# Kernel optimization log

Hardware: AMD Instinct MI355X
Metric: run time of the kernel (lower is better)

The kernel has to match this reference:

```python
import jax, jax.numpy as jnp
import numpy as np

B, N, T, H = 16, 512, 100, 64

def setup_inputs() -> dict:
    key = jax.random.key(0)
    ks = jax.random.split(key, 9)
    s = 0.1
    return {
        "x": jax.random.normal(ks[0], (B, N, T), dtype=jnp.float32),
        "conv1_w": jax.random.normal(ks[1], (16, 1, 3), dtype=jnp.float32) * s,
        "conv1_b": jax.random.normal(ks[2], (16,), dtype=jnp.float32) * s,
        "conv2_w": jax.random.normal(ks[3], (32, 16, 3), dtype=jnp.float32) * s,
        "conv2_b": jax.random.normal(ks[4], (32,), dtype=jnp.float32) * s,
        "W_ih": jax.random.normal(ks[5], (3 * H, 32), dtype=jnp.float32) * s,
        "W_hh": jax.random.normal(ks[6], (3 * H, H), dtype=jnp.float32) * s,
        "b_ih": jax.random.normal(ks[7], (3 * H,), dtype=jnp.float32) * s,
        "b_hh": jax.random.normal(ks[8], (3 * H,), dtype=jnp.float32) * s,
    }

def _causal_conv_relu(h, w, b):
    # h: [BN, C_in, T]; left-pad (k-1)*dilation = 2 for causality
    y = jax.lax.conv_general_dilated(
        h, w, window_strides=(1,), padding=[(2, 0)],
        dimension_numbers=("NCH", "OIH", "NCH"))
    return jax.nn.relu(y + b[None, :, None])

def reference(x, conv1_w, conv1_b, conv2_w, conv2_b, W_ih, W_hh, b_ih, b_hh):
    b_, n_, t_ = x.shape
    h = x.reshape(b_ * n_, 1, t_)
    h = _causal_conv_relu(h, conv1_w, conv1_b)   # [BN, 16, T]
    h = _causal_conv_relu(h, conv2_w, conv2_b)   # [BN, 32, T]
    seq = h.transpose(0, 2, 1)                   # [BN, T, 32]
    # precompute input-to-gate projections for all timesteps: [BN, T, 3H]
    xp = jnp.einsum("btc,gc->btg", seq, W_ih) + b_ih
    hdim = W_hh.shape[1]

    def step(hprev, xt):
        gh = hprev @ W_hh.T + b_hh               # [BN, 3H]
        xr, xz, xn = jnp.split(xt, 3, axis=-1)
        hr, hz, hn = jnp.split(gh, 3, axis=-1)
        r = jax.nn.sigmoid(xr + hr)
        z = jax.nn.sigmoid(xz + hz)
        nn_ = jnp.tanh(xn + r * hn)
        hnew = (1.0 - z) * nn_ + z * hprev
        return hnew, None

    h0 = jnp.zeros((b_ * n_, hdim), dtype=x.dtype)
    hf, _ = jax.lax.scan(step, h0, xp.transpose(1, 0, 2))  # scan over T
    return hf.reshape(b_, n_, hdim)
```

## Files before the change

### kernel.cpp

```cpp
#include <hip/hip_runtime.h>
#include <stdint.h>

typedef __attribute__((ext_vector_type(8))) short s16x8;
typedef __attribute__((ext_vector_type(4))) float f32x4;

__device__ __forceinline__ short f2bf(float f){
  union { float f; uint32_t u; } v; v.f = f;
  uint32_t u = v.u;
  u += 0x7fffu + ((u >> 16) & 1u);
  return (short)(u >> 16);
}
__device__ __forceinline__ float sigm_fast(float x){
  float e = __builtin_amdgcn_exp2f(x * -1.44269504f);
  return __builtin_amdgcn_rcpf(1.f + e);
}
__device__ __forceinline__ float tanh_fast(float x){
  float e = __builtin_amdgcn_exp2f(x * 2.88539008f);
  return __builtin_fmaf(-2.f, __builtin_amdgcn_rcpf(e + 1.f), 1.f);
}

#define MFMA16(a, b, c) __builtin_amdgcn_mfma_f32_16x16x32_bf16((a), (b), (c), 0, 0, 0)

__global__ __launch_bounds__(256, 2) void te_fused(
    const float* __restrict__ x,
    const float* __restrict__ w1, const float* __restrict__ b1,
    const float* __restrict__ w2, const float* __restrict__ b2,
    const float* __restrict__ Wih, const float* __restrict__ Whh,
    const float* __restrict__ bih, const float* __restrict__ bhh,
    float* __restrict__ out)
{
  constexpr int T = 100;
  constexpr int M = 16;
  __shared__ float x_s[M * T];
  __shared__ short hA[2][16 * 72];
  __shared__ short ring[4][16 * 24];
  __shared__ short s_s[2][16 * 40];

  const int tid  = threadIdx.x;
  const int lane = tid & 63;
  const int wv   = tid >> 6;
  const int l15  = lane & 15;
  const int lg   = lane >> 4;
  const int seq0 = blockIdx.x * M;
  const int sl   = tid >> 4;
  const int chc  = tid & 15;

  {
    const float4* gx = reinterpret_cast<const float4*>(x + (size_t)seq0 * T);
    float4* sx = reinterpret_cast<float4*>(x_s);
    for (int i = tid; i < (M * T) / 4; i += 256) sx[i] = gx[i];
  }
  {
    int* p = reinterpret_cast<int*>(&hA[0][0]);
    for (int i = tid; i < (16 * 72) / 2; i += 256) p[i] = 0;
    int* q = reinterpret_cast<int*>(&ring[0][0]);
    for (int i = tid; i < (4 * 16 * 24) / 2; i += 256) q[i] = 0;
  }

  s16x8 WhhHi[3][2], WihHi[3];
  f32x4 bias_r, bias_z, bias_xn, bias_hn;
#pragma unroll
  for (int g = 0; g < 3; ++g) {
    const int n = 64 * g + 16 * wv + l15;
#pragma unroll
    for (int ks = 0; ks < 2; ++ks) {
      const float* p = Whh + n * 64 + ks * 32 + lg * 8;
#pragma unroll
      for (int j = 0; j < 8; ++j) WhhHi[g][ks][j] = f2bf(p[j]);
    }
    const float* q = Wih + n * 32 + lg * 8;
#pragma unroll
    for (int j = 0; j < 8; ++j) WihHi[g][j] = f2bf(q[j]);
    float bi = bih[n], bh = bhh[n];
    if (g == 0) { float v = bi + bh; bias_r  = (f32x4){v, v, v, v}; }
    if (g == 1) { float v = bi + bh; bias_z  = (f32x4){v, v, v, v}; }
    if (g == 2) { bias_xn = (f32x4){bi, bi, bi, bi};
                  bias_hn = (f32x4){bh, bh, bh, bh}; }
  }

  s16x8 cW2[2];
  f32x4 b2v4;
  {
    const int nt = wv & 1;
    const int ch = 16 * nt + l15;
    float bv = b2[ch];
    b2v4 = (f32x4){bv, bv, bv, bv};
#pragma unroll
    for (int ks = 0; ks < 2; ++ks) {
      s16x8 h8;
#pragma unroll
      for (int j = 0; j < 8; ++j) {
        const int k = ks * 32 + lg * 8 + j;
        const int g = k >> 4, ii = k & 15;
        h8[j] = (g < 3) ? f2bf(w2[ch * 48 + ii * 3 + g]) : (short)0;
      }
      cW2[ks] = h8;
    }
  }

  const float w1v0 = w1[chc * 3 + 0], w1v1 = w1[chc * 3 + 1], w1v2 = w1[chc * 3 + 2];
  const float b1v = b1[chc];

  __syncthreads();

  float xa_r = x_s[sl * T + 0];
  float xb_r = x_s[sl * T + 1];

  const int i0a = (lg & 1) * 8;
  const int grp = lg >> 1;

  auto conv2_step = [&](int u, int buf) {
    const int sA0 = (u + 2 + grp) & 3;
    const int sA1 = (u + grp) & 3;
    s16x8 a0 = *reinterpret_cast<const s16x8*>(&ring[sA0][l15 * 24 + i0a]);
    s16x8 a1 = *reinterpret_cast<const s16x8*>(&ring[sA1][l15 * 24 + i0a]);
    f32x4 sa = MFMA16(a1, cW2[1], MFMA16(a0, cW2[0], b2v4));
    short* sw = &s_s[buf][0];
    float m0 = sa[0] > 0.f ? sa[0] : 0.f;
    float m1 = sa[1] > 0.f ? sa[1] : 0.f;
    float m2 = sa[2] > 0.f ? sa[2] : 0.f;
    float m3 = sa[3] > 0.f ? sa[3] : 0.f;
    uint32_t u01, u23;
    asm("v_cvt_pk_bf16_f32 %0, %1, %2" : "=v"(u01) : "v"(m0), "v"(m1));
    asm("v_cvt_pk_bf16_f32 %0, %1, %2" : "=v"(u23) : "v"(m2), "v"(m3));
    const int cbase = (wv & 1) * 16 + l15;
    sw[(lg * 4 + 0) * 40 + cbase] = (short)(u01 & 0xffff);
    sw[(lg * 4 + 1) * 40 + cbase] = (short)(u01 >> 16);
    sw[(lg * 4 + 2) * 40 + cbase] = (short)(u23 & 0xffff);
    sw[(lg * 4 + 3) * 40 + cbase] = (short)(u23 >> 16);
  };

  {
    float c = b1v + w1v2 * xa_r;
    c = c > 0.f ? c : 0.f;
    uint32_t cu;
    asm("v_cvt_pk_bf16_f32 %0, %1, %2" : "=v"(cu) : "v"(c), "v"(c));
    ring[0][sl * 24 + chc] = (short)(cu & 0xffff);
  }
  __syncthreads();
  if (wv < 2) conv2_step(0, 0);
  {
    float c = b1v + w1v1 * xa_r + w1v2 * xb_r;
    c = c > 0.f ? c : 0.f;
    uint32_t cu;
    asm("v_cvt_pk_bf16_f32 %0, %1, %2" : "=v"(cu) : "v"(c), "v"(c));
    ring[1][sl * 24 + chc] = (short)(cu & 0xffff);
  }
  __syncthreads();

  float hreg[4] = {0.f, 0.f, 0.f, 0.f};

  for (int t = 0; t < T; ++t) {
    s16x8 as_ = *reinterpret_cast<const s16x8*>(&s_s[t & 1][l15 * 40 + lg * 8]);
    const short* hb = &hA[t & 1][0];
    const int ho = l15 * 72 + lg * 8;
    s16x8 ah0 = *reinterpret_cast<const s16x8*>(hb + ho);
    s16x8 ah1 = *reinterpret_cast<const s16x8*>(hb + ho + 32);

    f32x4 pre_r = MFMA16(as_, WihHi[0],
                  MFMA16(ah1, WhhHi[0][1],
                  MFMA16(ah0, WhhHi[0][0], bias_r)));
    f32x4 pre_z = MFMA16(as_, WihHi[1],
                  MFMA16(ah1, WhhHi[1][1],
                  MFMA16(ah0, WhhHi[1][0], bias_z)));
    f32x4 xn = MFMA16(as_, WihHi[2], bias_xn);
    f32x4 hn = MFMA16(ah1, WhhHi[2][1],
               MFMA16(ah0, WhhHi[2][0], bias_hn));

    if (t < T - 1 && wv < 2) conv2_step(t + 1, (t + 1) & 1);

    if (t < T - 2) {
      float xc = x_s[sl * T + t + 2];
      float c = b1v + w1v0 * xa_r + w1v1 * xb_r + w1v2 * xc;
      c = c > 0.f ? c : 0.f;
      uint32_t cu;
      asm("v_cvt_pk_bf16_f32 %0, %1, %2" : "=v"(cu) : "v"(c), "v"(c));
      ring[(t + 2) & 3][sl * 24 + chc] = (short)(cu & 0xffff);
      xa_r = xb_r; xb_r = xc;
    }

    float hnew[4];
#pragma unroll
    for (int i2 = 0; i2 < 4; ++i2) {
      float r = sigm_fast(pre_r[i2]);
      float z = sigm_fast(pre_z[i2]);
      float arg = __builtin_fmaf(r, hn[i2], xn[i2]);
      float tn = tanh_fast(arg);
      float h = __builtin_fmaf(z, hreg[i2] - tn, tn);
      hreg[i2] = h;
      hnew[i2] = h;
    }
    short* hw = &hA[(t + 1) & 1][0];
    uint32_t p01, p23;
    asm("v_cvt_pk_bf16_f32 %0, %1, %2" : "=v"(p01) : "v"(hnew[0]), "v"(hnew[1]));
    asm("v_cvt_pk_bf16_f32 %0, %1, %2" : "=v"(p23) : "v"(hnew[2]), "v"(hnew[3]));
    const int hbase = 16 * wv + l15;
    hw[(lg * 4 + 0) * 72 + hbase] = (short)(p01 & 0xffff);
    hw[(lg * 4 + 1) * 72 + hbase] = (short)(p01 >> 16);
    hw[(lg * 4 + 2) * 72 + hbase] = (short)(p23 & 0xffff);
    hw[(lg * 4 + 3) * 72 + hbase] = (short)(p23 >> 16);
    __syncthreads();
  }

#pragma unroll
  for (int i2 = 0; i2 < 4; ++i2) {
    out[(size_t)(seq0 + lg * 4 + i2) * 64 + 16 * wv + l15] = hreg[i2];
  }
}

extern "C" void kernel_launch(void* const* d_in, const int* in_sizes, int n_in,
                              void* d_out, int out_size, void* d_ws, size_t ws_size,
                              hipStream_t stream)
{
  (void)in_sizes; (void)n_in; (void)d_ws; (void)ws_size; (void)out_size;
  const float* x   = (const float*)d_in[0];
  const float* w1  = (const float*)d_in[1];
  const float* b1  = (const float*)d_in[2];
  const float* w2  = (const float*)d_in[3];
  const float* b2  = (const float*)d_in[4];
  const float* Wih = (const float*)d_in[5];
  const float* Whh = (const float*)d_in[6];
  const float* bih = (const float*)d_in[7];
  const float* bhh = (const float*)d_in[8];
  float* out = (float*)d_out;
  te_fused<<<512, 256, 0, stream>>>(x, w1, b1, w2, b2, Wih, Whh, bih, bhh, out);
}
```

Measured before the change: 79.83 us.

## Unroll GRU loop by four, split conv work across waves, add MFMA priority

Unrolls the recurrent time loop by four so ring, h and s buffer offsets become compile-time constants, removing per-step index math and branch overhead. Conv1 work moves to waves 2-3 (two sequences per thread, packed bf16 convert) and conv2 stays on waves 0-1, so each wave does less side work on the critical path. Raises wave priority around the MFMA chain with s_setprio. The change adds code size and relies on precomputed offset arrays staying in registers.

```diff
diff --git a/kernel.cpp b/kernel.cpp
--- a/kernel.cpp
+++ b/kernel.cpp
@@ -42,8 +42,6 @@
   const int l15  = lane & 15;
   const int lg   = lane >> 4;
   const int seq0 = blockIdx.x * M;
-  const int sl   = tid >> 4;
-  const int chc  = tid & 15;
 
   {
     const float4* gx = reinterpret_cast<const float4*>(x + (size_t)seq0 * T);
@@ -81,8 +79,7 @@
   s16x8 cW2[2];
   f32x4 b2v4;
   {
-    const int nt = wv & 1;
-    const int ch = 16 * nt + l15;
+    const int ch = 16 * (wv & 1) + l15;
     float bv = b2[ch];
     b2v4 = (f32x4){bv, bv, bv, bv};
 #pragma unroll
@@ -98,109 +95,135 @@
     }
   }
 
-  const float w1v0 = w1[chc * 3 + 0], w1v1 = w1[chc * 3 + 1], w1v2 = w1[chc * 3 + 2];
-  const float b1v = b1[chc];
-
-  __syncthreads();
-
-  float xa_r = x_s[sl * T + 0];
-  float xb_r = x_s[sl * T + 1];
+  const int cidx = tid & 127;
+  const int csl  = cidx >> 4;
+  const int cch  = cidx & 15;
+  const float w1v0 = w1[cch * 3 + 0], w1v1 = w1[cch * 3 + 1], w1v2 = w1[cch * 3 + 2];
+  const float b1v = b1[cch];
 
   const int i0a = (lg & 1) * 8;
   const int grp = lg >> 1;
-
-  auto conv2_step = [&](int u, int buf) {
-    const int sA0 = (u + 2 + grp) & 3;
-    const int sA1 = (u + grp) & 3;
-    s16x8 a0 = *reinterpret_cast<const s16x8*>(&ring[sA0][l15 * 24 + i0a]);
-    s16x8 a1 = *reinterpret_cast<const s16x8*>(&ring[sA1][l15 * 24 + i0a]);
-    f32x4 sa = MFMA16(a1, cW2[1], MFMA16(a0, cW2[0], b2v4));
-    short* sw = &s_s[buf][0];
-    float m0 = sa[0] > 0.f ? sa[0] : 0.f;
-    float m1 = sa[1] > 0.f ? sa[1] : 0.f;
-    float m2 = sa[2] > 0.f ? sa[2] : 0.f;
-    float m3 = sa[3] > 0.f ? sa[3] : 0.f;
-    uint32_t u01, u23;
-    asm("v_cvt_pk_bf16_f32 %0, %1, %2" : "=v"(u01) : "v"(m0), "v"(m1));
-    asm("v_cvt_pk_bf16_f32 %0, %1, %2" : "=v"(u23) : "v"(m2), "v"(m3));
-    const int cbase = (wv & 1) * 16 + l15;
-    sw[(lg * 4 + 0) * 40 + cbase] = (short)(u01 & 0xffff);
-    sw[(lg * 4 + 1) * 40 + cbase] = (short)(u01 >> 16);
-    sw[(lg * 4 + 2) * 40 + cbase] = (short)(u23 & 0xffff);
-    sw[(lg * 4 + 3) * 40 + cbase] = (short)(u23 >> 16);
-  };
-
-  {
-    float c = b1v + w1v2 * xa_r;
-    c = c > 0.f ? c : 0.f;
+  const short* ringRdBase = &ring[0][0] + l15 * 24 + i0a;
+  int sA0off[4], sA1off[4];
+#pragma unroll
+  for (int p = 0; p < 4; ++p) {
+    sA0off[p] = ((p + 3 + grp) & 3) * 384;
+    sA1off[p] = ((p + 1 + grp) & 3) * 384;
+  }
+  const short* sRdBase = &s_s[0][0] + l15 * 40 + lg * 8;
+  const short* hRdBase = &hA[0][0] + l15 * 72 + lg * 8;
+  short* hWrBase = &hA[0][0] + (lg * 4) * 72 + 16 * wv + l15;
+  short* swWr    = &s_s[0][0] + (lg * 4) * 40 + (wv & 1) * 16 + l15;
+  short* ringWrA = &ring[0][0] + csl * 24 + cch;
+  short* ringWrB = &ring[0][0] + (csl + 8) * 24 + cch;
+  const float* xpA = &x_s[csl * T];
+  const float* xpB = &x_s[(csl + 8) * T];
+
+  __syncthreads();
+
+#define CONV2_STEP(P_, WB_) do {                                              \
+    s16x8 a0 = *reinterpret_cast<const s16x8*>(ringRdBase + sA0off[(P_)]);    \
+    s16x8 a1 = *reinterpret_cast<const s16x8*>(ringRdBase + sA1off[(P_)]);    \
+    f32x4 sa = MFMA16(a1, cW2[1], MFMA16(a0, cW2[0], b2v4));                  \
+    float m0 = sa[0] > 0.f ? sa[0] : 0.f;                                     \
+    float m1 = sa[1] > 0.f ? sa[1] : 0.f;                                     \
+    float m2 = sa[2] > 0.f ? sa[2] : 0.f;                                     \
+    float m3 = sa[3] > 0.f ? sa[3] : 0.f;                                     \
+    uint32_t u01, u23;                                                        \
+    asm("v_cvt_pk_bf16_f32 %0, %1, %2" : "=v"(u01) : "v"(m0), "v"(m1));       \
+    asm("v_cvt_pk_bf16_f32 %0, %1, %2" : "=v"(u23) : "v"(m2), "v"(m3));       \
+    swWr[(WB_) * 640 +   0] = (short)(u01 & 0xffff);                          \
+    swWr[(WB_) * 640 +  40] = (short)(u01 >> 16);                             \
+    swWr[(WB_) * 640 +  80] = (short)(u23 & 0xffff);                          \
+    swWr[(WB_) * 640 + 120] = (short)(u23 >> 16);                             \
+  } while (0)
+
+  float xaA = 0.f, xbA = 0.f, xaB = 0.f, xbB = 0.f;
+  if (wv >= 2) {
+    xaA = xpA[0]; xbA = xpA[1];
+    xaB = xpB[0]; xbB = xpB[1];
+    float cA = b1v + w1v2 * xaA; cA = cA > 0.f ? cA : 0.f;
+    float cB = b1v + w1v2 * xaB; cB = cB > 0.f ? cB : 0.f;
     uint32_t cu;
-    asm("v_cvt_pk_bf16_f32 %0, %1, %2" : "=v"(cu) : "v"(c), "v"(c));
-    ring[0][sl * 24 + chc] = (short)(cu & 0xffff);
+    asm("v_cvt_pk_bf16_f32 %0, %1, %2" : "=v"(cu) : "v"(cA), "v"(cB));
+    ringWrA[0] = (short)(cu & 0xffff);
+    ringWrB[0] = (short)(cu >> 16);
   }
   __syncthreads();
-  if (wv < 2) conv2_step(0, 0);
-  {
-    float c = b1v + w1v1 * xa_r + w1v2 * xb_r;
-    c = c > 0.f ? c : 0.f;
+  if (wv < 2) CONV2_STEP(3, 0);
+  if (wv >= 2) {
+    float cA = b1v + w1v1 * xaA + w1v2 * xbA; cA = cA > 0.f ? cA : 0.f;
+    float cB = b1v + w1v1 * xaB + w1v2 * xbB; cB = cB > 0.f ? cB : 0.f;
     uint32_t cu;
-    asm("v_cvt_pk_bf16_f32 %0, %1, %2" : "=v"(cu) : "v"(c), "v"(c));
-    ring[1][sl * 24 + chc] = (short)(cu & 0xffff);
+    asm("v_cvt_pk_bf16_f32 %0, %1, %2" : "=v"(cu) : "v"(cA), "v"(cB));
+    ringWrA[384] = (short)(cu & 0xffff);
+    ringWrB[384] = (short)(cu >> 16);
   }
   __syncthreads();
 
   float hreg[4] = {0.f, 0.f, 0.f, 0.f};
 
-  for (int t = 0; t < T; ++t) {
-    s16x8 as_ = *reinterpret_cast<const s16x8*>(&s_s[t & 1][l15 * 40 + lg * 8]);
-    const short* hb = &hA[t & 1][0];
-    const int ho = l15 * 72 + lg * 8;
-    s16x8 ah0 = *reinterpret_cast<const s16x8*>(hb + ho);
-    s16x8 ah1 = *reinterpret_cast<const s16x8*>(hb + ho + 32);
-
-    f32x4 pre_r = MFMA16(as_, WihHi[0],
-                  MFMA16(ah1, WhhHi[0][1],
-                  MFMA16(ah0, WhhHi[0][0], bias_r)));
-    f32x4 pre_z = MFMA16(as_, WihHi[1],
-                  MFMA16(ah1, WhhHi[1][1],
-                  MFMA16(ah0, WhhHi[1][0], bias_z)));
-    f32x4 xn = MFMA16(as_, WihHi[2], bias_xn);
-    f32x4 hn = MFMA16(ah1, WhhHi[2][1],
-               MFMA16(ah0, WhhHi[2][0], bias_hn));
-
-    if (t < T - 1 && wv < 2) conv2_step(t + 1, (t + 1) & 1);
-
-    if (t < T - 2) {
-      float xc = x_s[sl * T + t + 2];
-      float c = b1v + w1v0 * xa_r + w1v1 * xb_r + w1v2 * xc;
-      c = c > 0.f ? c : 0.f;
-      uint32_t cu;
-      asm("v_cvt_pk_bf16_f32 %0, %1, %2" : "=v"(cu) : "v"(c), "v"(c));
-      ring[(t + 2) & 3][sl * 24 + chc] = (short)(cu & 0xffff);
-      xa_r = xb_r; xb_r = xc;
-    }
-
-    float hnew[4];
-#pragma unroll
-    for (int i2 = 0; i2 < 4; ++i2) {
-      float r = sigm_fast(pre_r[i2]);
-      float z = sigm_fast(pre_z[i2]);
-      float arg = __builtin_fmaf(r, hn[i2], xn[i2]);
-      float tn = tanh_fast(arg);
-      float h = __builtin_fmaf(z, hreg[i2] - tn, tn);
-      hreg[i2] = h;
-      hnew[i2] = h;
-    }
-    short* hw = &hA[(t + 1) & 1][0];
-    uint32_t p01, p23;
-    asm("v_cvt_pk_bf16_f32 %0, %1, %2" : "=v"(p01) : "v"(hnew[0]), "v"(hnew[1]));
-    asm("v_cvt_pk_bf16_f32 %0, %1, %2" : "=v"(p23) : "v"(hnew[2]), "v"(hnew[3]));
-    const int hbase = 16 * wv + l15;
-    hw[(lg * 4 + 0) * 72 + hbase] = (short)(p01 & 0xffff);
-    hw[(lg * 4 + 1) * 72 + hbase] = (short)(p01 >> 16);
-    hw[(lg * 4 + 2) * 72 + hbase] = (short)(p23 & 0xffff);
-    hw[(lg * 4 + 3) * 72 + hbase] = (short)(p23 >> 16);
-    __syncthreads();
-  }
+#define GRU_STEP(T_, P_, C2_, C1_) do {                                       \
+    const int rb_ = (P_) & 1, wb_ = rb_ ^ 1;                                  \
+    s16x8 as_ = *reinterpret_cast<const s16x8*>(sRdBase + rb_ * 640);         \
+    s16x8 ah0 = *reinterpret_cast<const s16x8*>(hRdBase + rb_ * 1152);        \
+    s16x8 ah1 = *reinterpret_cast<const s16x8*>(hRdBase + rb_ * 1152 + 32);   \
+    __builtin_amdgcn_s_setprio(1);                                            \
+    f32x4 pre_r = MFMA16(as_, WihHi[0],                                       \
+                  MFMA16(ah1, WhhHi[0][1],                                    \
+                  MFMA16(ah0, WhhHi[0][0], bias_r)));                         \
+    f32x4 pre_z = MFMA16(as_, WihHi[1],                                       \
+                  MFMA16(ah1, WhhHi[1][1],                                    \
+                  MFMA16(ah0, WhhHi[1][0], bias_z)));                         \
+    f32x4 xn = MFMA16(as_, WihHi[2], bias_xn);                                \
+    f32x4 hn = MFMA16(ah1, WhhHi[2][1],                                       \
+               MFMA16(ah0, WhhHi[2][0], bias_hn));                            \
+    __builtin_amdgcn_s_setprio(0);                                            \
+    if ((C2_) && wv < 2) { CONV2_STEP((P_), wb_); }                           \
+    if ((C1_) && wv >= 2) {                                                   \
+      float xcA = xpA[(T_) + 2], xcB = xpB[(T_) + 2];                         \
+      float cA = b1v + w1v0 * xaA + w1v1 * xbA + w1v2 * xcA;                  \
+      cA = cA > 0.f ? cA : 0.f;                                               \
+      float cB = b1v + w1v0 * xaB + w1v1 * xbB + w1v2 * xcB;                  \
+      cB = cB > 0.f ? cB : 0.f;                                               \
+      uint32_t cu_;                                                           \
+      asm("v_cvt_pk_bf16_f32 %0, %1, %2" : "=v"(cu_) : "v"(cA), "v"(cB));     \
+      ringWrA[(((P_) + 2) & 3) * 384] = (short)(cu_ & 0xffff);                \
+      ringWrB[(((P_) + 2) & 3) * 384] = (short)(cu_ >> 16);                   \
+      xaA = xbA; xbA = xcA; xaB = xbB; xbB = xcB;                             \
+    }                                                                         \
+    float hnew[4];                                                            \
+    _Pragma("unroll")                                                         \
+    for (int i2 = 0; i2 < 4; ++i2) {                                          \
+      float r = sigm_fast(pre_r[i2]);                                         \
+      float z = sigm_fast(pre_z[i2]);                                         \
+      float arg = __builtin_fmaf(r, hn[i2], xn[i2]);                          \
+      float tn = tanh_fast(arg);                                              \
+      float h = __builtin_fmaf(z, hreg[i2] - tn, tn);                         \
+      hreg[i2] = h;                                                           \
+      hnew[i2] = h;                                                           \
+    }                                                                         \
+    uint32_t p01, p23;                                                        \
+    asm("v_cvt_pk_bf16_f32 %0, %1, %2" : "=v"(p01) : "v"(hnew[0]), "v"(hnew[1])); \
+    asm("v_cvt_pk_bf16_f32 %0, %1, %2" : "=v"(p23) : "v"(hnew[2]), "v"(hnew[3])); \
+    hWrBase[wb_ * 1152 +   0] = (short)(p01 & 0xffff);                        \
+    hWrBase[wb_ * 1152 +  72] = (short)(p01 >> 16);                           \
+    hWrBase[wb_ * 1152 + 144] = (short)(p23 & 0xffff);                        \
+    hWrBase[wb_ * 1152 + 216] = (short)(p23 >> 16);                           \
+    __syncthreads();                                                          \
+  } while (0)
+
+#pragma unroll 1
+  for (int t = 0; t < 96; t += 4) {
+    GRU_STEP(t + 0, 0, true, true);
+    GRU_STEP(t + 1, 1, true, true);
+    GRU_STEP(t + 2, 2, true, true);
+    GRU_STEP(t + 3, 3, true, true);
+  }
+  GRU_STEP(96, 0, true, true);
+  GRU_STEP(97, 1, true, true);
+  GRU_STEP(98, 2, true, false);
+  GRU_STEP(99, 3, false, false);
 
 #pragma unroll
   for (int i2 = 0; i2 < 4; ++i2) {
```

Result: faster. 74.11 us (-7.2%).

## Batch conv stages in 16-step chunks ahead of the GRU recurrence

Applied to the files above, without the earlier changes.

Replaces the per-timestep interleaved conv1/conv2 pipeline with chunked precomputation: every 16 timesteps, conv1 outputs for the chunk are written to shared memory, then all four waves compute conv2 for the chunk via MFMA, and then 16 fully unrolled GRU steps run using only the precomputed inputs. This takes conv work off the serial recurrence's critical path and adds s_setprio around the gate MFMAs. In exchange it uses much more LDS (about 27 KB more per block), which may reduce occupancy, and adds two extra barriers per chunk.

```diff
diff --git a/kernel.cpp b/kernel.cpp
--- a/kernel.cpp
+++ b/kernel.cpp
@@ -29,32 +29,26 @@
     const float* __restrict__ bih, const float* __restrict__ bhh,
     float* __restrict__ out)
 {
-  constexpr int T = 100;
-  constexpr int M = 16;
-  __shared__ float x_s[M * T];
+  __shared__ float x_s[16 * 100];
   __shared__ short hA[2][16 * 72];
-  __shared__ short ring[4][16 * 24];
-  __shared__ short s_s[2][16 * 40];
+  __shared__ short c1b[16 * 328];
+  __shared__ short s_b[16 * 640];
 
   const int tid  = threadIdx.x;
   const int lane = tid & 63;
   const int wv   = tid >> 6;
   const int l15  = lane & 15;
   const int lg   = lane >> 4;
-  const int seq0 = blockIdx.x * M;
-  const int sl   = tid >> 4;
-  const int chc  = tid & 15;
+  const int seq0 = blockIdx.x * 16;
 
   {
-    const float4* gx = reinterpret_cast<const float4*>(x + (size_t)seq0 * T);
+    const float4* gx = reinterpret_cast<const float4*>(x + (size_t)seq0 * 100);
     float4* sx = reinterpret_cast<float4*>(x_s);
-    for (int i = tid; i < (M * T) / 4; i += 256) sx[i] = gx[i];
+    for (int i = tid; i < 400; i += 256) sx[i] = gx[i];
   }
   {
     int* p = reinterpret_cast<int*>(&hA[0][0]);
-    for (int i = tid; i < (16 * 72) / 2; i += 256) p[i] = 0;
-    int* q = reinterpret_cast<int*>(&ring[0][0]);
-    for (int i = tid; i < (4 * 16 * 24) / 2; i += 256) q[i] = 0;
+    for (int i = tid; i < 576; i += 256) p[i] = 0;
   }
 
   s16x8 WhhHi[3][2], WihHi[3];
@@ -81,8 +75,7 @@
   s16x8 cW2[2];
   f32x4 b2v4;
   {
-    const int nt = wv & 1;
-    const int ch = 16 * nt + l15;
+    const int ch = 16 * (wv & 1) + l15;
     float bv = b2[ch];
     b2v4 = (f32x4){bv, bv, bv, bv};
 #pragma unroll
@@ -98,108 +91,116 @@
     }
   }
 
+  const int sl  = tid >> 4;
+  const int chc = tid & 15;
   const float w1v0 = w1[chc * 3 + 0], w1v1 = w1[chc * 3 + 1], w1v2 = w1[chc * 3 + 2];
   const float b1v = b1[chc];
 
+  const short* sRd  = &s_b[0]   + l15 * 40 + lg * 8;
+  const short* hRd  = &hA[0][0] + l15 * 72 + lg * 8;
+  short*       hWr  = &hA[0][0] + (lg * 4) * 72 + 16 * wv + l15;
+  const short* c1Rd = &c1b[0]   + l15 * 328 + lg * 8;
+  short*       sWr  = &s_b[0]   + (lg * 4) * 40 + (wv & 1) * 16 + l15;
+  short*       c1Wr = &c1b[0]   + sl * 328 + chc;
+  const float* xRd  = &x_s[sl * 100];
+  const int    ub   = (wv >> 1) * 8;
+
   __syncthreads();
 
-  float xa_r = x_s[sl * T + 0];
-  float xb_r = x_s[sl * T + 1];
-
-  const int i0a = (lg & 1) * 8;
-  const int grp = lg >> 1;
-
-  auto conv2_step = [&](int u, int buf) {
-    const int sA0 = (u + 2 + grp) & 3;
-    const int sA1 = (u + grp) & 3;
-    s16x8 a0 = *reinterpret_cast<const s16x8*>(&ring[sA0][l15 * 24 + i0a]);
-    s16x8 a1 = *reinterpret_cast<const s16x8*>(&ring[sA1][l15 * 24 + i0a]);
-    f32x4 sa = MFMA16(a1, cW2[1], MFMA16(a0, cW2[0], b2v4));
-    short* sw = &s_s[buf][0];
-    float m0 = sa[0] > 0.f ? sa[0] : 0.f;
-    float m1 = sa[1] > 0.f ? sa[1] : 0.f;
-    float m2 = sa[2] > 0.f ? sa[2] : 0.f;
-    float m3 = sa[3] > 0.f ? sa[3] : 0.f;
-    uint32_t u01, u23;
-    asm("v_cvt_pk_bf16_f32 %0, %1, %2" : "=v"(u01) : "v"(m0), "v"(m1));
-    asm("v_cvt_pk_bf16_f32 %0, %1, %2" : "=v"(u23) : "v"(m2), "v"(m3));
-    const int cbase = (wv & 1) * 16 + l15;
-    sw[(lg * 4 + 0) * 40 + cbase] = (short)(u01 & 0xffff);
-    sw[(lg * 4 + 1) * 40 + cbase] = (short)(u01 >> 16);
-    sw[(lg * 4 + 2) * 40 + cbase] = (short)(u23 & 0xffff);
-    sw[(lg * 4 + 3) * 40 + cbase] = (short)(u23 >> 16);
-  };
-
-  {
-    float c = b1v + w1v2 * xa_r;
-    c = c > 0.f ? c : 0.f;
-    uint32_t cu;
-    asm("v_cvt_pk_bf16_f32 %0, %1, %2" : "=v"(cu) : "v"(c), "v"(c));
-    ring[0][sl * 24 + chc] = (short)(cu & 0xffff);
-  }
-  __syncthreads();
-  if (wv < 2) conv2_step(0, 0);
-  {
-    float c = b1v + w1v1 * xa_r + w1v2 * xb_r;
-    c = c > 0.f ? c : 0.f;
-    uint32_t cu;
-    asm("v_cvt_pk_bf16_f32 %0, %1, %2" : "=v"(cu) : "v"(c), "v"(c));
-    ring[1][sl * 24 + chc] = (short)(cu & 0xffff);
-  }
-  __syncthreads();
-
   float hreg[4] = {0.f, 0.f, 0.f, 0.f};
 
-  for (int t = 0; t < T; ++t) {
-    s16x8 as_ = *reinterpret_cast<const s16x8*>(&s_s[t & 1][l15 * 40 + lg * 8]);
-    const short* hb = &hA[t & 1][0];
-    const int ho = l15 * 72 + lg * 8;
-    s16x8 ah0 = *reinterpret_cast<const s16x8*>(hb + ho);
-    s16x8 ah1 = *reinterpret_cast<const s16x8*>(hb + ho + 32);
-
-    f32x4 pre_r = MFMA16(as_, WihHi[0],
-                  MFMA16(ah1, WhhHi[0][1],
-                  MFMA16(ah0, WhhHi[0][0], bias_r)));
-    f32x4 pre_z = MFMA16(as_, WihHi[1],
-                  MFMA16(ah1, WhhHi[1][1],
-                  MFMA16(ah0, WhhHi[1][0], bias_z)));
-    f32x4 xn = MFMA16(as_, WihHi[2], bias_xn);
-    f32x4 hn = MFMA16(ah1, WhhHi[2][1],
-               MFMA16(ah0, WhhHi[2][0], bias_hn));
-
-    if (t < T - 1 && wv < 2) conv2_step(t + 1, (t + 1) & 1);
-
-    if (t < T - 2) {
-      float xc = x_s[sl * T + t + 2];
-      float c = b1v + w1v0 * xa_r + w1v1 * xb_r + w1v2 * xc;
-      c = c > 0.f ? c : 0.f;
-      uint32_t cu;
-      asm("v_cvt_pk_bf16_f32 %0, %1, %2" : "=v"(cu) : "v"(c), "v"(c));
-      ring[(t + 2) & 3][sl * 24 + chc] = (short)(cu & 0xffff);
-      xa_r = xb_r; xb_r = xc;
-    }
-
-    float hnew[4];
-#pragma unroll
-    for (int i2 = 0; i2 < 4; ++i2) {
-      float r = sigm_fast(pre_r[i2]);
-      float z = sigm_fast(pre_z[i2]);
-      float arg = __builtin_fmaf(r, hn[i2], xn[i2]);
-      float tn = tanh_fast(arg);
-      float h = __builtin_fmaf(z, hreg[i2] - tn, tn);
-      hreg[i2] = h;
-      hnew[i2] = h;
-    }
-    short* hw = &hA[(t + 1) & 1][0];
-    uint32_t p01, p23;
-    asm("v_cvt_pk_bf16_f32 %0, %1, %2" : "=v"(p01) : "v"(hnew[0]), "v"(hnew[1]));
-    asm("v_cvt_pk_bf16_f32 %0, %1, %2" : "=v"(p23) : "v"(hnew[2]), "v"(hnew[3]));
-    const int hbase = 16 * wv + l15;
-    hw[(lg * 4 + 0) * 72 + hbase] = (short)(p01 & 0xffff);
-    hw[(lg * 4 + 1) * 72 + hbase] = (short)(p01 >> 16);
-    hw[(lg * 4 + 2) * 72 + hbase] = (short)(p23 & 0xffff);
-    hw[(lg * 4 + 3) * 72 + hbase] = (short)(p23 >> 16);
+#define GSTEP(TL) do {                                                        \
+    const int rb_ = (TL) & 1, wb_ = rb_ ^ 1;                                  \
+    s16x8 as_ = *reinterpret_cast<const s16x8*>(sRd + (TL) * 640);            \
+    s16x8 ah0 = *reinterpret_cast<const s16x8*>(hRd + rb_ * 1152);            \
+    s16x8 ah1 = *reinterpret_cast<const s16x8*>(hRd + rb_ * 1152 + 32);       \
+    __builtin_amdgcn_s_setprio(1);                                            \
+    f32x4 pr = MFMA16(as_, WihHi[0],                                          \
+               MFMA16(ah1, WhhHi[0][1],                                       \
+               MFMA16(ah0, WhhHi[0][0], bias_r)));                            \
+    f32x4 pz = MFMA16(as_, WihHi[1],                                          \
+               MFMA16(ah1, WhhHi[1][1],                                       \
+               MFMA16(ah0, WhhHi[1][0], bias_z)));                            \
+    f32x4 xn = MFMA16(as_, WihHi[2], bias_xn);                                \
+    f32x4 hn = MFMA16(ah1, WhhHi[2][1],                                       \
+               MFMA16(ah0, WhhHi[2][0], bias_hn));                            \
+    __builtin_amdgcn_s_setprio(0);                                            \
+    float hnew[4];                                                            \
+    _Pragma("unroll")                                                         \
+    for (int i2 = 0; i2 < 4; ++i2) {                                          \
+      float r = sigm_fast(pr[i2]);                                            \
+      float z = sigm_fast(pz[i2]);                                            \
+      float tn = tanh_fast(__builtin_fmaf(r, hn[i2], xn[i2]));                \
+      float h = __builtin_fmaf(z, hreg[i2] - tn, tn);                         \
+      hreg[i2] = h; hnew[i2] = h;                                             \
+    }                                                                         \
+    uint32_t p01, p23;                                                        \
+    asm("v_cvt_pk_bf16_f32 %0, %1, %2" : "=v"(p01) : "v"(hnew[0]), "v"(hnew[1])); \
+    asm("v_cvt_pk_bf16_f32 %0, %1, %2" : "=v"(p23) : "v"(hnew[2]), "v"(hnew[3])); \
+    hWr[wb_ * 1152 +   0] = (short)(p01 & 0xffff);                            \
+    hWr[wb_ * 1152 +  72] = (short)(p01 >> 16);                               \
+    hWr[wb_ * 1152 + 144] = (short)(p23 & 0xffff);                            \
+    hWr[wb_ * 1152 + 216] = (short)(p23 >> 16);                               \
+    __syncthreads();                                                          \
+  } while (0)
+
+#pragma unroll 1
+  for (int k = 0; k < 7; ++k) {
+    const int t0 = k * 16;
+
+    {
+      int xi0 = t0 - 4, xi1 = t0 - 3;
+      float xa = (xi0 < 0) ? 0.f : xRd[xi0 < 0 ? 0 : xi0];
+      float xb = (xi1 < 0) ? 0.f : xRd[xi1 < 0 ? 0 : xi1];
+#pragma unroll
+      for (int i = 0; i < 19; ++i) {
+        const int xi = t0 - 2 + i;
+        const int idx = xi < 0 ? 0 : (xi > 99 ? 99 : xi);
+        float xv = xRd[idx];
+        float xc = (xi < 0) ? 0.f : xv;
+        float c = __builtin_fmaf(w1v0, xa,
+                  __builtin_fmaf(w1v1, xb,
+                  __builtin_fmaf(w1v2, xc, b1v)));
+        c = c > 0.f ? c : 0.f;
+        c = (xi < 0) ? 0.f : c;
+        uint32_t cu;
+        asm("v_cvt_pk_bf16_f32 %0, %1, %2" : "=v"(cu) : "v"(c), "v"(c));
+        c1Wr[i * 16] = (short)(cu & 0xffff);
+        xa = xb; xb = xc;
+      }
+    }
     __syncthreads();
+
+    {
+#pragma unroll
+      for (int i = 0; i < 8; ++i) {
+        const int u = ub + i;
+        s16x8 a0 = *reinterpret_cast<const s16x8*>(c1Rd + u * 16);
+        s16x8 a1 = *reinterpret_cast<const s16x8*>(c1Rd + u * 16 + 32);
+        f32x4 sa = MFMA16(a1, cW2[1], MFMA16(a0, cW2[0], b2v4));
+        float m0 = sa[0] > 0.f ? sa[0] : 0.f;
+        float m1 = sa[1] > 0.f ? sa[1] : 0.f;
+        float m2 = sa[2] > 0.f ? sa[2] : 0.f;
+        float m3 = sa[3] > 0.f ? sa[3] : 0.f;
+        uint32_t u01, u23;
+        asm("v_cvt_pk_bf16_f32 %0, %1, %2" : "=v"(u01) : "v"(m0), "v"(m1));
+        asm("v_cvt_pk_bf16_f32 %0, %1, %2" : "=v"(u23) : "v"(m2), "v"(m3));
+        sWr[u * 640 +   0] = (short)(u01 & 0xffff);
+        sWr[u * 640 +  40] = (short)(u01 >> 16);
+        sWr[u * 640 +  80] = (short)(u23 & 0xffff);
+        sWr[u * 640 + 120] = (short)(u23 >> 16);
+      }
+    }
+    __syncthreads();
+
+    if (k < 6) {
+      GSTEP(0);  GSTEP(1);  GSTEP(2);  GSTEP(3);
+      GSTEP(4);  GSTEP(5);  GSTEP(6);  GSTEP(7);
+      GSTEP(8);  GSTEP(9);  GSTEP(10); GSTEP(11);
+      GSTEP(12); GSTEP(13); GSTEP(14); GSTEP(15);
+    } else {
+      GSTEP(0);  GSTEP(1);  GSTEP(2);  GSTEP(3);
+    }
   }
 
 #pragma unroll
```

Measured after the change: 74.64 us. 1.07x faster.
